# Kernel tuning notes

Hardware: AMD Instinct MI355X
Metric: run time of the kernel (lower is better)

The kernel has to match this reference:

```python
import jax, jax.numpy as jnp
import numpy as np

B, C, H, W = 8, 256, 128, 128
NH, WS = 8, 8
HD = C // NH
WNH, WNW = H // WS, W // WS


def _rel_pos_index():
    coords = np.stack(np.meshgrid(np.arange(WS), np.arange(WS), indexing='ij'))  # [2,ws,ws]
    flat = coords.reshape(2, -1)
    rel = (flat[:, :, None] - flat[:, None, :]).transpose(1, 2, 0)  # [ws^2,ws^2,2]
    rel[..., 0] += WS - 1
    rel[..., 1] += WS - 1
    rel[..., 0] *= 2 * WS - 1
    return jnp.asarray(rel.sum(-1))  # [ws^2,ws^2]


def grid_sample(img, grid):
    # Bilinear, padding_mode='zeros', align_corners=True. img [N,C,H,W], grid [N,Hg,Wg,2] (x,y in [-1,1])
    N, Ci, Hi, Wi = img.shape
    gx = (grid[..., 0] + 1.0) * 0.5 * (Wi - 1)
    gy = (grid[..., 1] + 1.0) * 0.5 * (Hi - 1)
    x0 = jnp.floor(gx)
    y0 = jnp.floor(gy)
    x0i = x0.astype(jnp.int32)
    y0i = y0.astype(jnp.int32)
    wx1 = gx - x0
    wx0 = 1.0 - wx1
    wy1 = gy - y0
    wy0 = 1.0 - wy1
    nb = jnp.arange(N)[:, None, None]

    def corner(yi, xi, wgt):
        valid = (yi >= 0) & (yi < Hi) & (xi >= 0) & (xi < Wi)
        yc = jnp.clip(yi, 0, Hi - 1)
        xc = jnp.clip(xi, 0, Wi - 1)
        val = img[nb, :, yc, xc]  # [N,Hg,Wg,C]
        return val * (wgt * valid)[..., None]

    out = (corner(y0i, x0i, wy0 * wx0) + corner(y0i, x0i + 1, wy0 * wx1)
           + corner(y0i + 1, x0i, wy1 * wx0) + corner(y0i + 1, x0i + 1, wy1 * wx1))
    return jnp.transpose(out, (0, 3, 1, 2))


def setup_inputs() -> dict:
    key = jax.random.key(0)
    ks = jax.random.split(key, 10)
    f = lambda k, s, sc=1.0: jax.random.normal(k, s, dtype=jnp.float32) * sc
    return {
        'x': f(ks[0], (B, C, H, W)),
        'qkv_w': f(ks[1], (3 * C, C), 0.02),
        'qkv_b': f(ks[2], (3 * C,), 0.02),
        'bias_w': f(ks[3], (2 * NH, C), 0.02),
        'bias_b': f(ks[4], (2 * NH,), 0.02),
        'scale_w': f(ks[5], (2 * NH, C), 0.02),
        'scale_b': f(ks[6], (2 * NH,), 0.02),
        'proj_w': f(ks[7], (C, C), 0.02),
        'proj_b': f(ks[8], (C,), 0.02),
        'rpb_table': f(ks[9], ((2 * WS - 1) ** 2, NH), 0.02),
    }


def reference(x, qkv_w, qkv_b, bias_w, bias_b, scale_w, scale_b, proj_w, proj_b, rpb_table):
    scale = HD ** -0.5
    N = B * NH
    # ---- deterministic base sampling coordinates (shift=0, no padding since H,W % WS == 0) ----
    lin_w = jnp.linspace(-1.0, 1.0, W)
    lin_h = jnp.linspace(-1.0, 1.0, H)
    winref_w = lin_w.reshape(WNW, WS).mean(-1)  # window centers along width
    winref_h = lin_h.reshape(WNH, WS).mean(-1)
    off_w = jnp.arange(WS) * 2.0 / (W - 1)
    off_w = off_w - off_w.mean()
    off_h = jnp.arange(WS) * 2.0 / (H - 1)
    off_h = off_h - off_h.mean()
    base_x = jnp.broadcast_to(winref_w[None, None, :, None] + off_w[None, None, None, :], (WNH, WS, WNW, WS))
    base_y = jnp.broadcast_to((winref_h[:, None] + off_h[None, :])[:, :, None, None], (WNH, WS, WNW, WS))
    # ---- predicted per-head per-window biases & scales ----
    xp = jax.nn.leaky_relu(x.reshape(B, C, WNH, WS, WNW, WS).mean((3, 5)))  # [B,C,WNH,WNW]
    biases = (jnp.einsum('oc,bchw->bohw', bias_w, xp) + bias_b[None, :, None, None]).reshape(N, 2, WNH, WNW)
    bx = biases[:, 0] / WNW  # sampling_biases[:,0] / (w // ws)
    by = biases[:, 1] / WNH
    scales = (jnp.einsum('oc,bchw->bohw', scale_w, xp) + scale_b[None, :, None, None]).reshape(N, 2, WNH, WNW)
    sx, sy = scales[:, 0], scales[:, 1]
    # final = base + local_offsets * scale + bias (broadcast [N,WNH,1,WNW,1] over window interior)
    cx = base_x[None] + off_w[None, None, None, None, :] * sx[:, :, None, :, None] + bx[:, :, None, :, None]
    cy = base_y[None] + off_h[None, None, :, None, None] * sy[:, :, None, :, None] + by[:, :, None, :, None]
    grid = jnp.stack([cx, cy], -1).reshape(N, H, W, 2)
    # ---- qkv via 1x1 conv ----
    qkv = (jnp.einsum('oc,bchw->bohw', qkv_w, x) + qkv_b[None, :, None, None]).reshape(B, 3, NH, HD, H, W)
    q = qkv[:, 0].reshape(N, HD, H, W)
    k = qkv[:, 1].reshape(N, HD, H, W)
    v = qkv[:, 2].reshape(N, HD, H, W)
    ksamp = grid_sample(k, grid)
    vsamp = grid_sample(v, grid)

    def win(t):  # [N,HD,H,W] -> [B, nWin, NH, WS*WS, HD]
        t = t.reshape(B, NH, HD, WNH, WS, WNW, WS)
        return jnp.transpose(t, (0, 3, 5, 1, 4, 6, 2)).reshape(B, WNH * WNW, NH, WS * WS, HD)

    qw, kw, vw = win(q), win(ksamp), win(vsamp)
    rpb = jnp.transpose(rpb_table[_rel_pos_index().reshape(-1)].reshape(WS * WS, WS * WS, NH), (2, 0, 1))
    attn = jnp.einsum('bwhqd,bwhkd->bwhqk', qw, kw) * scale + rpb[None, None]
    attn = jax.nn.softmax(attn, axis=-1)
    out = jnp.einsum('bwhqk,bwhkd->bwhqd', attn, vw)
    out = out.reshape(B, WNH, WNW, NH, WS, WS, HD)
    out = jnp.transpose(out, (0, 3, 6, 1, 4, 2, 5)).reshape(B, C, H, W)
    out = jnp.einsum('oc,bchw->bohw', proj_w, out) + proj_b[None, :, None, None]
    return out
```

## Files before the change

### kernel.cpp

```cpp
#include <hip/hip_runtime.h>
#include <hip/hip_fp16.h>

#define B_ 8
#define C_ 256
#define H_ 128
#define W_ 128
#define NH_ 8
#define WS_ 8
#define HD_ 32
#define WN_ 16
#define NWIN_ 256
#define HW_ 16384

typedef unsigned short ushort_t;
typedef unsigned int uint_t;
typedef __attribute__((ext_vector_type(8))) short short8;
typedef _Float16 __attribute__((ext_vector_type(8))) half8;
typedef __attribute__((ext_vector_type(4))) float f32x4;

__device__ __forceinline__ ushort_t bf16_rtn(float x) {
    uint_t u = __float_as_uint(x);
    return (ushort_t)((u + 0x7FFFu + ((u >> 16) & 1u)) >> 16);
}
__device__ __forceinline__ uint_t bfpack(float a, float b) {
    return (uint_t)bf16_rtn(a) | ((uint_t)bf16_rtn(b) << 16);
}
__device__ __forceinline__ uint_t h2pack(float a, float b) {
    __half2 h = __floats2half2_rn(a, b);
    return __builtin_bit_cast(uint_t, h);
}

__global__ __launch_bounds__(256) void wpack_kernel(const float* __restrict__ w,
                            ushort_t* __restrict__ wpk) {
    int u = blockIdx.x*256 + threadIdx.x;
    int lane = u & 63;
    int f    = (u >> 6) & 3;
    int kk   = (u >> 8) & 1;
    int ks   = (u >> 9) & 3;
    int wm   = (u >> 11) & 1;
    int oc   = u >> 12;
    int o = oc*128 + wm*64 + f*16 + (lane & 15);
    int c = ks*64 + kk*32 + (lane >> 4)*8;
    const float* src = w + (size_t)o*256 + c;
    float4 v0 = *(const float4*)src;
    float4 v1 = *(const float4*)(src + 4);
    uint4 Hv;
    Hv.x = bfpack(v0.x, v0.y); Hv.y = bfpack(v0.z, v0.w);
    Hv.z = bfpack(v1.x, v1.y); Hv.w = bfpack(v1.z, v1.w);
    ((uint4*)wpk)[u] = Hv;
}

__global__ __launch_bounds__(256) void wconv_kernel(const float* __restrict__ w,
                            ushort_t* __restrict__ wh, int n4) {
    int i = blockIdx.x*256 + threadIdx.x;
    if (i >= n4) return;
    float4 v = ((const float4*)w)[i];
    ((uint2*)wh)[i] = make_uint2(bfpack(v.x, v.y), bfpack(v.z, v.w));
}

__global__ __launch_bounds__(256) void rpb_expand_kernel(const float* __restrict__ rpb_table,
                            float* __restrict__ rpbT) {
    int nh = blockIdx.x;
    int t = threadIdx.x;
    #pragma unroll
    for (int rr = 0; rr < 16; ++rr) {
        int e = t*16 + rr;
        int kcol = e >> 6, qrow = e & 63;
        int yq = qrow >> 3, xq = qrow & 7, yk = kcol >> 3, xk = kcol & 7;
        int idx = (yq - yk + 7)*15 + (xq - xk + 7);
        rpbT[((size_t)nh*64 + kcol)*64 + qrow] = rpb_table[idx*8 + nh];
    }
}

__global__ __launch_bounds__(256) void transpose_split_kernel(const float* __restrict__ x,
                            ushort_t* __restrict__ th, float* __restrict__ xpart) {
    __shared__ float tile[64][65];
    int b = blockIdx.z;
    int p0 = blockIdx.x * 64, c0 = blockIdx.y * 64;
    const float* xsrc = x + (size_t)b*C_*HW_;
    int t = threadIdx.x;
    #pragma unroll
    for (int r = 0; r < 4; ++r) {
        int task = t + r*256;
        int cl = task >> 4, p4 = (task & 15) * 4;
        float4 v = *(const float4*)(xsrc + (size_t)(c0+cl)*HW_ + p0 + p4);
        tile[cl][p4+0] = v.x; tile[cl][p4+1] = v.y; tile[cl][p4+2] = v.z; tile[cl][p4+3] = v.w;
    }
    __syncthreads();
    {
        int h = blockIdx.x >> 1, wbase = (blockIdx.x & 1) * 8;
        #pragma unroll
        for (int r = 0; r < 2; ++r) {
            int task = t + r*256;
            int cl = task >> 3, wx = task & 7;
            float s = 0.f;
            #pragma unroll
            for (int j = 0; j < 8; ++j) s += tile[cl][wx*8+j];
            xpart[(((size_t)b*256 + c0+cl)*128 + h)*16 + wbase + wx] = s;
        }
    }
    ushort_t* thb = th + (size_t)b*HW_*256;
    #pragma unroll
    for (int r = 0; r < 2; ++r) {
        int task = t + r*256;
        int pl = task >> 3, cb = (task & 7) * 8;
        uint4 Hh;
        Hh.x = bfpack(tile[cb+0][pl], tile[cb+1][pl]);
        Hh.y = bfpack(tile[cb+2][pl], tile[cb+3][pl]);
        Hh.z = bfpack(tile[cb+4][pl], tile[cb+5][pl]);
        Hh.w = bfpack(tile[cb+6][pl], tile[cb+7][pl]);
        *(uint4*)(thb + (size_t)(p0+pl)*256 + c0 + cb) = Hh;
    }
}

__global__ __launch_bounds__(256) void pool2_kernel(const float* __restrict__ xpart, float* __restrict__ xp) {
    int bc = blockIdx.x;
    int t = threadIdx.x;
    int wy = t >> 4, wxg = t & 15;
    const float* src = xpart + (size_t)bc*2048;
    float s = 0.f;
    #pragma unroll
    for (int i = 0; i < 8; ++i) s += src[(wy*8+i)*16 + wxg];
    s *= (1.f/64.f);
    xp[(size_t)bc*256 + t] = s > 0.f ? s : 0.01f*s;
}

__global__ __launch_bounds__(256) void params_kernel(const float* __restrict__ xp,
                              const float* __restrict__ bias_w, const float* __restrict__ bias_b,
                              const float* __restrict__ scale_w, const float* __restrict__ scale_b,
                              float* __restrict__ params) {
    __shared__ float xs[256];
    int blk = blockIdx.x;
    int b = blk >> 8, win = blk & 255;
    int t = threadIdx.x;
    xs[t] = xp[((size_t)(b*256 + t))*256 + win];
    __syncthreads();
    if (t < 32) {
        int which = t >> 4;
        int o = t & 15;
        const float* Wm = which ? scale_w : bias_w;
        float acc = which ? scale_b[o] : bias_b[o];
        for (int c = 0; c < 256; ++c) acc += Wm[o*256 + c] * xs[c];
        int nh = o >> 1, comp = o & 1;
        int n = b*8 + nh;
        float v = which ? acc : 3.96875f * acc;
        params[((size_t)(n*256 + win))*4 + which*2 + comp] = v;
    }
}

__global__ __launch_bounds__(256) void mgemm_qkvt2_kernel(const ushort_t* __restrict__ wpk,
                            const ushort_t* __restrict__ xt,
                            const float* __restrict__ bias,
                            ushort_t* __restrict__ qt, ushort_t* __restrict__ kv) {
    __shared__ __align__(16) float smem_f[64*67];
    uint4* Bh = (uint4*)smem_f;
    float* tb = smem_f;
    int zb = blockIdx.z;
    int oc = blockIdx.x;
    int o0 = oc * 128, p0 = blockIdx.y * 128;
    const ushort_t* xh = xt + (size_t)zb*HW_*256;
    ushort_t* qtb = qt + (size_t)zb*HW_*256;
    ushort_t* kvb = kv + (size_t)zb*8*HW_*64;
    int t = threadIdx.x;
    int lane = t & 63, wid = t >> 6;
    int wm = wid >> 1, wn = wid & 1;
    int qi = lane >> 4, rl = lane & 15;

    const ushort_t* wpkA = wpk + (size_t)(oc*2 + wm)*16384;

    f32x4 acc[4][4];
    #pragma unroll
    for (int f = 0; f < 4; ++f)
        #pragma unroll
        for (int g = 0; g < 4; ++g)
            acc[f][g] = (f32x4){0.f, 0.f, 0.f, 0.f};

    int srow = t >> 1, shalf = t & 1;
    int sw = srow & 7;

    for (int ks = 0; ks < 4; ++ks) {
        __syncthreads();
        {
            const uint4* src = (const uint4*)(xh + (size_t)(p0+srow)*256 + ks*64);
            #pragma unroll
            for (int jj = 0; jj < 4; ++jj) {
                int u = shalf*4 + jj;
                Bh[srow*8 + (u ^ sw)] = src[u];
            }
        }
        __syncthreads();
        #pragma unroll
        for (int kk = 0; kk < 2; ++kk) {
            short8 afh[4], bfh[4];
            const ushort_t* wk = wpkA + ((ks*2 + kk)*4)*512 + lane*8;
            #pragma unroll
            for (int f = 0; f < 4; ++f)
                afh[f] = *(const short8*)(wk + f*512);
            #pragma unroll
            for (int g = 0; g < 4; ++g) {
                int row = wn*64 + g*16 + rl;
                int u = (kk*4 + qi) ^ (row & 7);
                bfh[g] = __builtin_bit_cast(short8, Bh[row*8 + u]);
            }
            #pragma unroll
            for (int f = 0; f < 4; ++f)
                #pragma unroll
                for (int g = 0; g < 4; ++g)
                    acc[f][g] = __builtin_amdgcn_mfma_f32_16x16x32_bf16(afh[f], bfh[g], acc[f][g], 0, 0, 0);
        }
    }
    #pragma unroll
    for (int pm = 0; pm < 2; ++pm) {
        #pragma unroll
        for (int pn = 0; pn < 2; ++pn) {
            __syncthreads();
            if (wm == pm && wn == pn) {
                #pragma unroll
                for (int f = 0; f < 4; ++f)
                    #pragma unroll
                    for (int g = 0; g < 4; ++g)
                        #pragma unroll
                        for (int r = 0; r < 4; ++r)
                            tb[(f*16 + qi*4 + r)*67 + g*16 + rl] = acc[f][g][r];
            }
            __syncthreads();
            {
                int pxl = t >> 2, cg = t & 3;
                size_t pix = p0 + pn*64 + pxl;
                int obase = o0 + pm*64 + cg*16;
                int type = obase >> 8;
                int oo = obase & 255;
                int head = oo >> 5;
                ushort_t* dst = (type == 0)
                    ? qtb + pix*256 + oo
                    : kvb + ((size_t)head*HW_ + pix)*64 + ((type == 2) ? 32 : 0) + (oo & 31);
                float v[16];
                #pragma unroll
                for (int e = 0; e < 16; ++e) v[e] = tb[(cg*16 + e)*67 + pxl];
                float4 b0 = *(const float4*)&bias[obase];
                float4 b1 = *(const float4*)&bias[obase + 4];
                float4 b2 = *(const float4*)&bias[obase + 8];
                float4 b3 = *(const float4*)&bias[obase + 12];
                uint4 H0, H1;
                H0.x = h2pack(v[0]+b0.x,  v[1]+b0.y);  H0.y = h2pack(v[2]+b0.z,  v[3]+b0.w);
                H0.z = h2pack(v[4]+b1.x,  v[5]+b1.y);  H0.w = h2pack(v[6]+b1.z,  v[7]+b1.w);
                H1.x = h2pack(v[8]+b2.x,  v[9]+b2.y);  H1.y = h2pack(v[10]+b2.z, v[11]+b2.w);
                H1.z = h2pack(v[12]+b3.x, v[13]+b3.y); H1.w = h2pack(v[14]+b3.z, v[15]+b3.w);
                *(uint4*)dst = H0;
                *(uint4*)(dst + 8) = H1;
            }
        }
    }
}

__global__ __launch_bounds__(256) void mgemm_proj_kernel(const ushort_t* __restrict__ wp,
                            const ushort_t* __restrict__ at,
                            const float* __restrict__ bias, float* __restrict__ out) {
    __shared__ __align__(16) uint4 smem[2048];
    uint4* Ah = smem; uint4* Bh = smem + 1024;
    int zb = blockIdx.z;
    const ushort_t* xh = at + (size_t)zb*HW_*256;
    float* outb = out + (size_t)zb*C_*HW_;
    int o0 = blockIdx.x * 128, p0 = blockIdx.y * 128;
    int t = threadIdx.x;
    int lane = t & 63, wid = t >> 6;
    int wm = wid >> 1, wn = wid & 1;
    int q = lane >> 4, rl = lane & 15;

    f32x4 acc[4][4];
    #pragma unroll
    for (int f = 0; f < 4; ++f)
        #pragma unroll
        for (int g = 0; g < 4; ++g)
            acc[f][g] = (f32x4){0.f, 0.f, 0.f, 0.f};

    int srow = t >> 1, shalf = t & 1;
    int sw = srow & 7;

    for (int ks = 0; ks < 4; ++ks) {
        int c0 = ks * 64;
        __syncthreads();
        {
            const uint4* a_h = (const uint4*)(wp + (size_t)(o0+srow)*256 + c0);
            const uint4* b_h = (const uint4*)(xh + (size_t)(p0+srow)*256 + c0);
            #pragma unroll
            for (int jj = 0; jj < 4; ++jj) {
                int u = shalf*4 + jj;
                int d = srow*8 + (u ^ sw);
                Ah[d] = a_h[u]; Bh[d] = b_h[u];
            }
        }
        __syncthreads();
        #pragma unroll
        for (int kk = 0; kk < 2; ++kk) {
            short8 afh[4], bfh[4];
            #pragma unroll
            for (int f = 0; f < 4; ++f) {
                int row = wm*64 + f*16 + rl;
                int u = (kk*4 + q) ^ (row & 7);
                afh[f] = __builtin_bit_cast(short8, Ah[row*8 + u]);
            }
            #pragma unroll
            for (int g = 0; g < 4; ++g) {
                int row = wn*64 + g*16 + rl;
                int u = (kk*4 + q) ^ (row & 7);
                bfh[g] = __builtin_bit_cast(short8, Bh[row*8 + u]);
            }
            #pragma unroll
            for (int f = 0; f < 4; ++f)
                #pragma unroll
                for (int g = 0; g < 4; ++g)
                    acc[f][g] = __builtin_amdgcn_mfma_f32_16x16x32_bf16(afh[f], bfh[g], acc[f][g], 0, 0, 0);
        }
    }
    #pragma unroll
    for (int f = 0; f < 4; ++f) {
        float4 bb = *(const float4*)&bias[o0 + wm*64 + f*16 + q*4];
        float bbv[4] = {bb.x, bb.y, bb.z, bb.w};
        #pragma unroll
        for (int g = 0; g < 4; ++g) {
            int p = p0 + wn*64 + g*16 + rl;
            #pragma unroll
            for (int r = 0; r < 4; ++r) {
                int o = o0 + wm*64 + f*16 + q*4 + r;
                outb[(size_t)o*HW_ + p] = acc[f][g][r] + bbv[r];
            }
        }
    }
}

__global__ __launch_bounds__(256) void attn_kernel(const ushort_t* __restrict__ qt,
                            const ushort_t* __restrict__ kv,
                            const float* __restrict__ params_,
                            const float* __restrict__ rpbT,
                            ushort_t* __restrict__ at) {
    __shared__ __align__(16) ushort_t smem[64*40 + 64*40 + 32*72 + 64*40];
    ushort_t (*Q_lds)[40]   = (ushort_t(*)[40])smem;
    ushort_t (*K_lds)[40]   = (ushort_t(*)[40])(smem + 2560);
    ushort_t (*VT_lds)[72]  = (ushort_t(*)[72])(smem + 5120);
    ushort_t (*P_lds)[72]   = (ushort_t(*)[72])smem;
    ushort_t (*OUT_lds)[40] = (ushort_t(*)[40])(smem + 5120 + 2304);

    int b = blockIdx.y;
    int blk = blockIdx.x;
    int win = blk >> 3, nh = blk & 7;
    int wy = win >> 4, wx = win & 15;
    int t = threadIdx.x;
    int lane = t & 63, wid = t >> 6;

    const float* pp = params_ + ((size_t)((b*8 + nh)*256 + win))*4;
    float ox = pp[0], oy = pp[1], sx = pp[2], sy = pp[3];

    const ushort_t* qtb = qt + (size_t)b*HW_*256;
    const ushort_t* kvb = kv + ((size_t)(b*8 + nh))*HW_*64;
    ushort_t* ath = at + (size_t)b*HW_*256;

    {
        int tok = t >> 2, cg = t & 3;
        int i = tok >> 3, j = tok & 7;
        size_t pix = (size_t)(wy*8 + i)*W_ + wx*8 + j;
        *(uint4*)&Q_lds[tok][cg*8] = *(const uint4*)(qtb + pix*256 + nh*32 + cg*8);
    }
    {
        int tokq = lane >> 3, sub = lane & 7;
        #pragma unroll
        for (int r = 0; r < 2; ++r) {
            int tok = wid*16 + r*8 + tokq;
            int i = tok >> 3, j = tok & 7;
            int h = wy*8 + i, wpx = wx*8 + j;
            float gx = (float)wpx + ((float)j - 3.5f)*sx + ox;
            float gy = (float)h  + ((float)i - 3.5f)*sy + oy;
            float x0f = floorf(gx), y0f = floorf(gy);
            int x0 = (int)x0f, y0 = (int)y0f;
            float wx1 = gx - x0f, wy1 = gy - y0f;
            float wxz = 1.f - wx1, wyz = 1.f - wy1;
            int x1 = x0 + 1, y1 = y0 + 1;
            float m00 = wyz*wxz * ((y0>=0 && y0<H_ && x0>=0 && x0<W_) ? 1.f : 0.f);
            float m01 = wyz*wx1 * ((y0>=0 && y0<H_ && x1>=0 && x1<W_) ? 1.f : 0.f);
            float m10 = wy1*wxz * ((y1>=0 && y1<H_ && x0>=0 && x0<W_) ? 1.f : 0.f);
            float m11 = wy1*wx1 * ((y1>=0 && y1<H_ && x1>=0 && x1<W_) ? 1.f : 0.f);
            int x0c = min(max(x0,0),W_-1), x1c = min(max(x1,0),W_-1);
            int y0c = min(max(y0,0),H_-1), y1c = min(max(y1,0),H_-1);
            size_t p00 = (size_t)y0c*W_ + x0c, p01 = (size_t)y0c*W_ + x1c;
            size_t p10 = (size_t)y1c*W_ + x0c, p11 = (size_t)y1c*W_ + x1c;
            __half2 a0 = __float2half2_rn(0.f), a1 = a0, a2 = a0, a3 = a0;
            #define CORNER(PIX, M) { \
                uint4 u = *(const uint4*)(kvb + (PIX)*64 + sub*8); \
                __half2 wv = __float2half2_rn(M); \
                a0 = __hfma2(__builtin_bit_cast(__half2, u.x), wv, a0); \
                a1 = __hfma2(__builtin_bit_cast(__half2, u.y), wv, a1); \
                a2 = __hfma2(__builtin_bit_cast(__half2, u.z), wv, a2); \
                a3 = __hfma2(__builtin_bit_cast(__half2, u.w), wv, a3); }
            CORNER(p00, m00)
            CORNER(p01, m01)
            CORNER(p10, m10)
            CORNER(p11, m11)
            #undef CORNER
            if (sub < 4) {
                uint4 Kv;
                Kv.x = __builtin_bit_cast(uint_t, a0); Kv.y = __builtin_bit_cast(uint_t, a1);
                Kv.z = __builtin_bit_cast(uint_t, a2); Kv.w = __builtin_bit_cast(uint_t, a3);
                *(uint4*)&K_lds[tok][sub*8] = Kv;
            } else {
                int d0 = (sub - 4)*8;
                VT_lds[d0+0][tok] = __half_as_ushort(__low2half(a0));
                VT_lds[d0+1][tok] = __half_as_ushort(__high2half(a0));
                VT_lds[d0+2][tok] = __half_as_ushort(__low2half(a1));
                VT_lds[d0+3][tok] = __half_as_ushort(__high2half(a1));
                VT_lds[d0+4][tok] = __half_as_ushort(__low2half(a2));
                VT_lds[d0+5][tok] = __half_as_ushort(__high2half(a2));
                VT_lds[d0+6][tok] = __half_as_ushort(__low2half(a3));
                VT_lds[d0+7][tok] = __half_as_ushort(__high2half(a3));
            }
        }
    }
    __syncthreads();

    int q = lane >> 4, rl = lane & 15;
    const float scale = 0.17677669529663687f;

    half8 a_frag = *(const half8*)&Q_lds[wid*16 + rl][q*8];
    half8 b_frag[4];
    #pragma unroll
    for (int g = 0; g < 4; ++g)
        b_frag[g] = *(const half8*)&K_lds[g*16 + rl][q*8];
    __syncthreads();

    f32x4 accS[4];
    #pragma unroll
    for (int g = 0; g < 4; ++g)
        accS[g] = __builtin_amdgcn_mfma_f32_16x16x32_f16(a_frag, b_frag[g], (f32x4){0.f,0.f,0.f,0.f}, 0, 0, 0);

    float Sv[4][4];
    const float* rpbb = rpbT + (size_t)nh*4096;
    int m0 = wid*16 + q*4;
    #pragma unroll
    for (int g = 0; g < 4; ++g) {
        float4 rv = *(const float4*)&rpbb[(g*16 + rl)*64 + m0];
        Sv[g][0] = accS[g][0]*scale + rv.x;
        Sv[g][1] = accS[g][1]*scale + rv.y;
        Sv[g][2] = accS[g][2]*scale + rv.z;
        Sv[g][3] = accS[g][3]*scale + rv.w;
    }
    float inv[4];
    #pragma unroll
    for (int r = 0; r < 4; ++r) {
        float pm = fmaxf(fmaxf(Sv[0][r], Sv[1][r]), fmaxf(Sv[2][r], Sv[3][r]));
        pm = fmaxf(pm, __shfl_xor(pm, 1));
        pm = fmaxf(pm, __shfl_xor(pm, 2));
        pm = fmaxf(pm, __shfl_xor(pm, 4));
        pm = fmaxf(pm, __shfl_xor(pm, 8));
        float s = 0.f;
        #pragma unroll
        for (int g = 0; g < 4; ++g) {
            float e = __expf(Sv[g][r] - pm);
            Sv[g][r] = e;
            s += e;
        }
        s += __shfl_xor(s, 1);
        s += __shfl_xor(s, 2);
        s += __shfl_xor(s, 4);
        s += __shfl_xor(s, 8);
        inv[r] = 1.f / s;
    }
    #pragma unroll
    for (int r = 0; r < 4; ++r) {
        int m = wid*16 + q*4 + r;
        #pragma unroll
        for (int g = 0; g < 4; ++g)
            P_lds[m][g*16 + rl] = __half_as_ushort(__float2half(Sv[g][r]*inv[r]));
    }

    f32x4 accO[2] = {(f32x4){0.f,0.f,0.f,0.f}, (f32x4){0.f,0.f,0.f,0.f}};
    #pragma unroll
    for (int ks = 0; ks < 2; ++ks) {
        half8 p_frag = *(const half8*)&P_lds[wid*16 + rl][ks*32 + q*8];
        #pragma unroll
        for (int g2 = 0; g2 < 2; ++g2) {
            half8 v_frag = *(const half8*)&VT_lds[g2*16 + rl][ks*32 + q*8];
            accO[g2] = __builtin_amdgcn_mfma_f32_16x16x32_f16(p_frag, v_frag, accO[g2], 0, 0, 0);
        }
    }
    #pragma unroll
    for (int r = 0; r < 4; ++r) {
        int m = wid*16 + q*4 + r;
        OUT_lds[m][rl]      = bf16_rtn(accO[0][r]);
        OUT_lds[m][16 + rl] = bf16_rtn(accO[1][r]);
    }
    __syncthreads();
    {
        int tok = t >> 2, cg = t & 3;
        int i2 = tok >> 3, j2 = tok & 7;
        size_t pix = (size_t)(wy*8 + i2)*W_ + wx*8 + j2;
        *(uint4*)(ath + pix*256 + nh*32 + cg*8) = *(const uint4*)&OUT_lds[tok][cg*8];
    }
}

extern "C" void kernel_launch(void* const* d_in, const int* in_sizes, int n_in,
                              void* d_out, int out_size, void* d_ws, size_t ws_size,
                              hipStream_t stream) {
    const float* x       = (const float*)d_in[0];
    const float* qkv_w   = (const float*)d_in[1];
    const float* qkv_b   = (const float*)d_in[2];
    const float* bias_w  = (const float*)d_in[3];
    const float* bias_b  = (const float*)d_in[4];
    const float* scale_w = (const float*)d_in[5];
    const float* scale_b = (const float*)d_in[6];
    const float* proj_w  = (const float*)d_in[7];
    const float* proj_b  = (const float*)d_in[8];
    const float* rpb     = (const float*)d_in[9];
    float* out = (float*)d_out;

    char* ws = (char*)d_ws;
    float*    xp       = (float*)ws;     ws += (size_t)524288*4;
    float*    params   = (float*)ws;     ws += (size_t)65536*4;
    float*    xpart    = (float*)ws;     ws += (size_t)4194304*4;
    float*    rpbT     = (float*)ws;     ws += (size_t)8*4096*4;
    ushort_t* wpk      = (ushort_t*)ws;  ws += (size_t)768*256*2;
    ushort_t* wp       = (ushort_t*)ws;  ws += (size_t)256*256*2;
    ushort_t* xt       = (ushort_t*)ws;  ws += (size_t)B_*HW_*256*2;
    ushort_t* at       = (ushort_t*)ws;  ws += (size_t)B_*HW_*256*2;
    ushort_t* qt       = (ushort_t*)ws;  ws += (size_t)B_*HW_*256*2;
    ushort_t* kv       = (ushort_t*)ws;

    wpack_kernel<<<dim3(96), 256, 0, stream>>>(qkv_w, wpk);
    wconv_kernel<<<dim3(64), 256, 0, stream>>>(proj_w, wp, 256*256/4);
    rpb_expand_kernel<<<dim3(NH_), 256, 0, stream>>>(rpb, rpbT);
    transpose_split_kernel<<<dim3(256, 4, B_), 256, 0, stream>>>(x, xt, xpart);
    pool2_kernel <<<dim3(B_*C_), 256, 0, stream>>>(xpart, xp);
    params_kernel<<<dim3(B_*NWIN_), 256, 0, stream>>>(xp, bias_w, bias_b, scale_w, scale_b, params);
    mgemm_qkvt2_kernel<<<dim3(6, 128, B_), 256, 0, stream>>>(wpk, xt, qkv_b, qt, kv);
    attn_kernel<<<dim3(NH_*NWIN_, B_), 256, 0, stream>>>(qt, kv, params, rpbT, at);
    mgemm_proj_kernel<<<dim3(2, 128, B_), 256, 0, stream>>>(wp, at, proj_b, out);
}
```

Measured before the change: 362.5 us.

## Double-buffer QKV GEMM B tiles with direct global-to-LDS async loads

The QKV projection GEMM now stages its activation tiles with global_load_lds (direct global-to-LDS DMA) into two LDS buffers. The next K-slice is prefetched while MFMAs run on the current one, using vmcnt waits and raw s_barrier in place of the old load-then-sync loop. This targets the load latency exposed between K steps. LDS use grows to two 16KB buffers, which may lower occupancy, and the swizzle and wait counts must line up exactly for correctness.

```diff
diff --git a/kernel.cpp b/kernel.cpp
--- a/kernel.cpp
+++ b/kernel.cpp
@@ -28,6 +28,12 @@
 __device__ __forceinline__ uint_t h2pack(float a, float b) {
     __half2 h = __floats2half2_rn(a, b);
     return __builtin_bit_cast(uint_t, h);
+}
+__device__ __forceinline__ void gload_lds16(const void* g, void* l) {
+    __builtin_amdgcn_global_load_lds(
+        (const __attribute__((address_space(1))) unsigned int*)g,
+        (__attribute__((address_space(3))) unsigned int*)l,
+        16, 0, 0);
 }
 
 __global__ __launch_bounds__(256) void wpack_kernel(const float* __restrict__ w,
@@ -148,13 +154,11 @@
     }
 }
 
-__global__ __launch_bounds__(256) void mgemm_qkvt2_kernel(const ushort_t* __restrict__ wpk,
+__global__ __launch_bounds__(256) void mgemm_qkvt3_kernel(const ushort_t* __restrict__ wpk,
                             const ushort_t* __restrict__ xt,
                             const float* __restrict__ bias,
                             ushort_t* __restrict__ qt, ushort_t* __restrict__ kv) {
-    __shared__ __align__(16) float smem_f[64*67];
-    uint4* Bh = (uint4*)smem_f;
-    float* tb = smem_f;
+    __shared__ __align__(16) uint4 Bbuf[2][1024];
     int zb = blockIdx.z;
     int oc = blockIdx.x;
     int o0 = oc * 128, p0 = blockIdx.y * 128;
@@ -175,20 +179,30 @@
         for (int g = 0; g < 4; ++g)
             acc[f][g] = (f32x4){0.f, 0.f, 0.f, 0.f};
 
-    int srow = t >> 1, shalf = t & 1;
-    int sw = srow & 7;
-
+    auto STAGE = [&](int ks, int bsel) {
+        #pragma unroll
+        for (int i = 0; i < 4; ++i) {
+            int s = (wid*4 + i)*64 + lane;
+            int row = s >> 3;
+            int u = (s & 7) ^ (row & 7);
+            const ushort_t* g = xh + (size_t)(p0+row)*256 + ks*64 + u*8;
+            gload_lds16(g, &Bbuf[bsel][(wid*4 + i)*64]);
+        }
+    };
+
+    STAGE(0, 0);
+    #pragma unroll
     for (int ks = 0; ks < 4; ++ks) {
-        __syncthreads();
-        {
-            const uint4* src = (const uint4*)(xh + (size_t)(p0+srow)*256 + ks*64);
-            #pragma unroll
-            for (int jj = 0; jj < 4; ++jj) {
-                int u = shalf*4 + jj;
-                Bh[srow*8 + (u ^ sw)] = src[u];
-            }
-        }
-        __syncthreads();
+        int cur = ks & 1;
+        if (ks < 3) {
+            STAGE(ks+1, cur ^ 1);
+            asm volatile("s_waitcnt vmcnt(4)" ::: "memory");
+        } else {
+            asm volatile("s_waitcnt vmcnt(0)" ::: "memory");
+        }
+        __builtin_amdgcn_sched_barrier(0);
+        __builtin_amdgcn_s_barrier();
+        uint4* Bh = Bbuf[cur];
         #pragma unroll
         for (int kk = 0; kk < 2; ++kk) {
             short8 afh[4], bfh[4];
@@ -208,7 +222,10 @@
                 for (int g = 0; g < 4; ++g)
                     acc[f][g] = __builtin_amdgcn_mfma_f32_16x16x32_bf16(afh[f], bfh[g], acc[f][g], 0, 0, 0);
         }
-    }
+        __builtin_amdgcn_s_barrier();
+    }
+
+    float* tb = (float*)&Bbuf[0][0];
     #pragma unroll
     for (int pm = 0; pm < 2; ++pm) {
         #pragma unroll
@@ -529,7 +546,7 @@
     transpose_split_kernel<<<dim3(256, 4, B_), 256, 0, stream>>>(x, xt, xpart);
     pool2_kernel <<<dim3(B_*C_), 256, 0, stream>>>(xpart, xp);
     params_kernel<<<dim3(B_*NWIN_), 256, 0, stream>>>(xp, bias_w, bias_b, scale_w, scale_b, params);
-    mgemm_qkvt2_kernel<<<dim3(6, 128, B_), 256, 0, stream>>>(wpk, xt, qkv_b, qt, kv);
+    mgemm_qkvt3_kernel<<<dim3(6, 128, B_), 256, 0, stream>>>(wpk, xt, qkv_b, qt, kv);
     attn_kernel<<<dim3(NH_*NWIN_, B_), 256, 0, stream>>>(qt, kv, params, rpbT, at);
     mgemm_proj_kernel<<<dim3(2, 128, B_), 256, 0, stream>>>(wp, at, proj_b, out);
 }
```

Measured after the change: 364.8 us. No clear change (+0.6%).
